# Kernel tuning notes

Hardware: AMD Instinct MI355X
Metric: run time of the kernel (lower is better)

Reference implementation:

```python
import jax, jax.numpy as jnp
import numpy as np

# ---- constants from init_kwargs (mode='local', channel='G') ----
MEAN = 127.5
STD = 50.0
BINS = np.array([-2.4, -1.6, -0.8, 0.0, 0.8, 1.6, 2.4])
NB = len(BINS) + 1            # 8 quantization levels
DIST = [1, 2, 3]
THETA = [0.0, np.pi / 4, np.pi / 2, 3 * np.pi / 4]
MASK = 17
STRIDE = 4
BIN_EDGES = 0.5 + BINS / 6.0
# skimage greycomatrix offsets: (round(sin(t)*d), round(cos(t)*d)), ordered d-major
OFFSETS = [(int(np.round(np.sin(t) * d)), int(np.round(np.cos(t) * d)))
           for d in DIST for t in THETA]


def setup_inputs() -> dict:
    key = jax.random.key(0)
    x = jax.random.uniform(key, (8, 3, 256, 256), dtype=jnp.float32) * 255.0
    return {"x": x}


def _features(x):
    img = x[:, 1, :, :]                       # channel 'G'
    img = jnp.where(img < 10.0, 0.0, img)     # imgs[imgs < 10] = 0
    B, H, W = img.shape
    N = (H - MASK) // STRIDE + 1              # 60 windows per axis

    # sliding windows -> (B, N, N, MASK, MASK)
    r = (jnp.arange(N) * STRIDE)[:, None] + jnp.arange(MASK)[None, :]
    win = img[:, r[:, None, :, None], r[None, :, None, :]]
    Nw = B * N * N
    flat = win.reshape(Nw, MASK * MASK)

    # ---- stat over nonzero pixels (numpy population std) ----
    mask = flat != 0.0
    n_safe = jnp.maximum(mask.sum(-1), 1).astype(flat.dtype)
    mean = jnp.where(mask, flat, 0.0).sum(-1) / n_safe
    std = jnp.sqrt((jnp.where(mask, flat - mean[:, None], 0.0) ** 2).sum(-1) / n_safe)
    mx = jnp.where(mask, flat, -jnp.inf).max(-1)
    mn = jnp.where(mask, flat, jnp.inf).min(-1)
    stat = jnp.stack([mean, std, (mx - mean) / (std + 1e-9), (mean - mn) / (std + 1e-9)], -1)

    # ---- quantize ----
    q = jnp.digitize(((flat - MEAN) / STD + 3.0) / 6.0, jnp.asarray(BIN_EDGES, flat.dtype))

    # ---- histogram (density over ALL pixels, drop first & last bin) ----
    onehot = (q[..., None] == jnp.arange(NB)).astype(flat.dtype)
    hist_feat = onehot.sum(1)[:, 1:NB - 1] / flat.shape[1]   # (Nw, len(BINS)-1)

    # ---- GLCM per (dist, theta) offset, symmetric + normed ----
    qm = q.reshape(Nw, MASK, MASK)
    rows = jnp.arange(Nw)[:, None]
    glcms = []
    for dr, dc in OFFSETS:
        if dc >= 0:
            i = qm[:, :MASK - dr, :MASK - dc]
            j = qm[:, dr:, dc:]
        else:
            i = qm[:, :MASK - dr, -dc:]
            j = qm[:, dr:, :MASK + dc]
        pair = (i * NB + j).reshape(Nw, -1)
        cnt = jnp.zeros((Nw, NB * NB), flat.dtype).at[rows, pair].add(1.0)
        P = cnt.reshape(Nw, NB, NB)
        P = P + P.transpose(0, 2, 1)                               # symmetric
        P = P / jnp.maximum(P.sum((1, 2), keepdims=True), 1e-12)   # normed
        glcms.append(P)
    G = jnp.stack(glcms, 1)          # (Nw, 12, NB, NB)
    g = G[:, :, 1:, 1:]              # crop level 0 (zeros)
    L = NB - 1

    # greycoprops renormalizes the (cropped) GLCM internally
    Pn = g / jnp.maximum(g.sum((2, 3), keepdims=True), 1e-12)
    I = jnp.arange(L, dtype=flat.dtype)
    diff2 = (I[:, None] - I[None, :]) ** 2
    contrast = (Pn * diff2).sum((2, 3))
    homog = (Pn / (1.0 + diff2)).sum((2, 3))
    energy = jnp.sqrt((Pn ** 2).sum((2, 3)))
    Pi = Pn.sum(3)
    Pj = Pn.sum(2)
    mui = (Pi * I).sum(-1)
    muj = (Pj * I).sum(-1)
    sdi = jnp.sqrt((Pi * (I - mui[..., None]) ** 2).sum(-1))
    sdj = jnp.sqrt((Pj * (I - muj[..., None]) ** 2).sum(-1))
    cov = (Pn * (I[:, None] - mui[..., None, None]) * (I[None, :] - muj[..., None, None])).sum((2, 3))
    corr = jnp.where(sdi * sdj < 1e-15, 1.0, cov / jnp.maximum(sdi * sdj, 1e-15))
    entropy = -(g * jnp.log2(g + 1e-8)).sum((2, 3))   # on cropped, non-renormed g

    glcm_feat = jnp.concatenate([contrast, homog, energy, corr, entropy], -1)  # (Nw, 60)
    feats = jnp.concatenate([stat, hist_feat, glcm_feat], -1)                  # (Nw, 70)

    # windows with max == 0 yield all-zero feature vectors
    feats = jnp.where((flat.max(-1) == 0.0)[:, None], 0.0, feats)

    Fdim = feats.shape[-1]
    feats = feats.reshape(B, N, N, Fdim)
    total = feats.sum((1, 2))
    nz = (feats != 0).sum((1, 2)).astype(flat.dtype)
    return total / (nz + 1e-9)            # (B, 70)


def reference(x):
    return _features(x)
```

## Files before the change

kernel.cpp:

```cpp
#include <hip/hip_runtime.h>
#include <cmath>

#define NPIX   289
#define NU     10
#define NF     70
#define NWX    60
#define IMG_W  256
#define IMG_HW 65536
#define NWIN   28800
#define ACC    560
#define WPB    2
#define NBLK   (NWIN / WPB)
#define GLS    29

__device__ __constant__ int c_s2u[12] = {0,1,2,3,4,1,5,3,6,7,8,9};

constexpr int JOFF[NU] = {1, 18, 17, 16, 2, 34, 3, 36, 51, 32};
constexpr float INV2N[NU] = {1.f/544.f, 1.f/512.f, 1.f/544.f, 1.f/512.f, 1.f/510.f,
                             1.f/510.f, 1.f/476.f, 1.f/450.f, 1.f/476.f, 1.f/450.f};

struct CMs { unsigned m[10]; };
constexpr CMs mkcm(int dc) {
    CMs c{};
    for (int t = 0; t < NPIX; ++t) {
        int col = t % 17;
        bool ok = (dc > 0) ? (col >= dc) : (col <= 16 + dc);
        if (ok) c.m[t >> 5] |= 1u << (t & 31);
    }
    return c;
}
constexpr CMs CMp1 = mkcm(1), CMp2 = mkcm(2), CMp3 = mkcm(3);
constexpr CMs CMn1 = mkcm(-1), CMn2 = mkcm(-2);

struct alignas(32) FtE { float w, d2, inv, si, sii, sij, q0, q1; };
struct FtTab { FtE e[28]; };
constexpr FtTab mkft() {
    FtTab t{};
    int n = 0;
    for (int a = 1; a <= 7; ++a)
        for (int b = a; b <= 7; ++b) {
            int i = a - 1, j = b - 1;
            float w  = (a == b) ? 1.f : 2.f;
            float d2 = (float)((i - j) * (i - j));
            t.e[n] = FtE{w, d2, 1.f / (1.f + d2),
                         0.5f * (float)(i + j),
                         0.5f * (float)(i * i + j * j),
                         (float)(i * j), 0.f, 0.f};
            ++n;
        }
    return t;
}
__device__ __constant__ FtTab c_ft = mkft();

template<int O>
__device__ __forceinline__ int gcnt(const unsigned* __restrict__ M,
                                    const unsigned* __restrict__ ma) {
    constexpr int wq = JOFF[O] >> 5;
    constexpr int rr = JOFF[O] & 31;
    constexpr int nw = (288 - JOFF[O]) / 32 + 1;
    int acc = 0;
#pragma unroll
    for (int w = 0; w < nw; ++w) {
        unsigned sh = (rr == 0) ? M[w + wq]
                                : __builtin_amdgcn_alignbit(M[w + wq + 1], M[w + wq], rr);
        acc += __popc(ma[w] & sh);
    }
    return acc;
}

#define DPP_F(oldv, srcv, ctrl, rm) \
    __int_as_float(__builtin_amdgcn_update_dpp((oldv), __float_as_int(srcv), (ctrl), (rm), 0xF, false))

__device__ __forceinline__ float dpp_wsum(float v) {
    v += DPP_F(0, v, 0x111, 0xF);
    v += DPP_F(0, v, 0x112, 0xF);
    v += DPP_F(0, v, 0x114, 0xF);
    v += DPP_F(0, v, 0x118, 0xF);
    v += DPP_F(0, v, 0x142, 0xA);
    v += DPP_F(0, v, 0x143, 0xC);
    return __int_as_float(__builtin_amdgcn_readlane(__float_as_int(v), 63));
}
__device__ __forceinline__ float dpp_wmax(float v) {
    v = fmaxf(v, DPP_F(__float_as_int(v), v, 0x111, 0xF));
    v = fmaxf(v, DPP_F(__float_as_int(v), v, 0x112, 0xF));
    v = fmaxf(v, DPP_F(__float_as_int(v), v, 0x114, 0xF));
    v = fmaxf(v, DPP_F(__float_as_int(v), v, 0x118, 0xF));
    v = fmaxf(v, DPP_F(__float_as_int(v), v, 0x142, 0xA));
    v = fmaxf(v, DPP_F(__float_as_int(v), v, 0x143, 0xC));
    return __int_as_float(__builtin_amdgcn_readlane(__float_as_int(v), 63));
}
__device__ __forceinline__ float dpp_wmin(float v) {
    v = fminf(v, DPP_F(__float_as_int(v), v, 0x111, 0xF));
    v = fminf(v, DPP_F(__float_as_int(v), v, 0x112, 0xF));
    v = fminf(v, DPP_F(__float_as_int(v), v, 0x114, 0xF));
    v = fminf(v, DPP_F(__float_as_int(v), v, 0x118, 0xF));
    v = fminf(v, DPP_F(__float_as_int(v), v, 0x142, 0xA));
    v = fminf(v, DPP_F(__float_as_int(v), v, 0x143, 0xC));
    return __int_as_float(__builtin_amdgcn_readlane(__float_as_int(v), 63));
}

__device__ __forceinline__ float bperm_f(int addr, float v) {
    return __int_as_float(__builtin_amdgcn_ds_bpermute(addr, __float_as_int(v)));
}

__global__ __launch_bounds__(128, 8) void feat_kernel(const float* __restrict__ x,
                                                      float* __restrict__ ptot,
                                                      float* __restrict__ pnz,
                                                      int setmask) {
    __shared__ float s_g[WPB][NU * GLS];
    __shared__ float s_uf[WPB][5][NU];
    __shared__ float s_s10[WPB][10];

    const int lane = threadIdx.x & 63;
    const int wid  = threadIdx.x >> 6;
    const int widx = blockIdx.x * WPB + wid;
    const int b    = widx / 3600;
    const int rem  = widx - b * 3600;
    const int wy   = rem / NWX;
    const int wx   = rem - wy * NWX;
    const float* img = x + (size_t)(b * 3 + 1) * IMG_HW + (wy * 4) * IMG_W + wx * 4;

    float* gl  = s_g[wid];
    float (*uf)[NU] = s_uf[wid];
    float* s10 = s_s10[wid];

    const int l49 = (lane < 49) ? lane : 48;
    const int ba  = l49 / 7 + 1;
    const int bb  = l49 - (ba - 1) * 7 + 1;
    const int partner = (bb - 1) * 7 + (ba - 1);
    const int paddr   = partner << 2;
    const unsigned long long xm0a = (ba & 1) ? 0ull : ~0ull;
    const unsigned long long xm1a = (ba & 2) ? 0ull : ~0ull;
    const unsigned long long xm2a = (ba & 4) ? 0ull : ~0ull;

    float lsum = 0.f, lss = 0.f, lmax = -1e30f, lmin = 1e30f;
    int n = 0, c1 = 0, c2 = 0, c3 = 0, c4 = 0, c5 = 0, c6 = 0;
    unsigned ma32[10];
#pragma unroll
    for (int k = 0; k < 5; ++k) {
        const int t = lane + k * 64;
        float val;
        if (k < 4) {
            const int r = t / 17;
            float p = img[r * (IMG_W - 17) + t];
            val = (p < 10.f) ? 0.f : p;
        } else {
            float p = 0.f;
            if (t < NPIX) {
                const int r = t / 17;
                p = img[r * (IMG_W - 17) + t];
            }
            val = (p < 10.f) ? 0.f : p;
        }
        int qq = (int)fmaf(val, 0.025f, 0.8125f);
        lsum += val;
        float d = (val != 0.f) ? (val - 127.5f) : 0.f;
        lss = fmaf(d, d, lss);
        lmax = fmaxf(lmax, val);
        lmin = fminf(lmin, (val != 0.f) ? val : 1e30f);
        unsigned long long p0 = __ballot(qq & 1);
        unsigned long long p1 = __ballot(qq & 2);
        unsigned long long p2 = __ballot(qq & 4);
        n  += __popcll(p0 | p1 | p2);
        c1 += __popcll(p0 & ~p1 & ~p2);
        c2 += __popcll(~p0 & p1 & ~p2);
        c3 += __popcll(p0 & p1 & ~p2);
        c4 += __popcll(~p0 & ~p1 & p2);
        c5 += __popcll(p0 & ~p1 & p2);
        c6 += __popcll(~p0 & p1 & p2);
        unsigned long long mA = (p0 ^ xm0a) & (p1 ^ xm1a) & (p2 ^ xm2a);
        ma32[2*k]   = (unsigned)mA;
        ma32[2*k+1] = (unsigned)(mA >> 32);
    }

    if (n == 0) return;

    unsigned mv0[10];
#pragma unroll
    for (int w = 0; w < 10; ++w)
        mv0[w] = (unsigned)__builtin_amdgcn_ds_bpermute(paddr, (int)ma32[w]);

    const float fn   = (float)n;
    const float sum  = dpp_wsum(lsum);
    const float ss   = dpp_wsum(lss);
    const float mx   = dpp_wmax(lmax);
    const float mn   = dpp_wmin(lmin);
    const float mean = sum / fn;
    const float mc   = mean - 127.5f;
    const float var  = fmaxf(ss / fn - mc * mc, 0.f);
    const float stdv = sqrtf(var);

    if (lane == 0) {
        s10[0] = mean;
        s10[1] = stdv;
        s10[2] = (mx - mean) / (stdv + 1e-9f);
        s10[3] = (mean - mn) / (stdv + 1e-9f);
        s10[4] = (float)c1 * (1.f / 289.f);
        s10[5] = (float)c2 * (1.f / 289.f);
        s10[6] = (float)c3 * (1.f / 289.f);
        s10[7] = (float)c4 * (1.f / 289.f);
        s10[8] = (float)c5 * (1.f / 289.f);
        s10[9] = (float)c6 * (1.f / 289.f);
    }

    int cnta[NU];
    {
        cnta[2] = gcnt<2>(mv0, ma32);
        cnta[5] = gcnt<5>(mv0, ma32);
        cnta[8] = gcnt<8>(mv0, ma32);
        unsigned mv[10];
#pragma unroll
        for (int w = 0; w < 10; ++w) mv[w] = mv0[w] & CMp1.m[w];
        cnta[0] = gcnt<0>(mv, ma32);
        cnta[1] = gcnt<1>(mv, ma32);
#pragma unroll
        for (int w = 0; w < 10; ++w) mv[w] = mv0[w] & CMp2.m[w];
        cnta[4] = gcnt<4>(mv, ma32);
        cnta[7] = gcnt<7>(mv, ma32);
#pragma unroll
        for (int w = 0; w < 10; ++w) mv[w] = mv0[w] & CMp3.m[w];
        cnta[6] = gcnt<6>(mv, ma32);
#pragma unroll
        for (int w = 0; w < 10; ++w) mv[w] = mv0[w] & CMn1.m[w];
        cnta[3] = gcnt<3>(mv, ma32);
#pragma unroll
        for (int w = 0; w < 10; ++w) mv[w] = mv0[w] & CMn2.m[w];
        cnta[9] = gcnt<9>(mv, ma32);
    }

    const int amin  = min(ba, bb);
    const int idx28 = 8 * (amin - 1) - ((amin * (amin - 1)) >> 1) + (max(ba, bb) - amin);
    const bool wr   = (lane < 49) && (ba <= bb);
#pragma unroll
    for (int o = 0; o < NU; ++o) {
        int pc = __builtin_amdgcn_ds_bpermute(paddr, cnta[o]);
        float g = (float)(cnta[o] + pc) * INV2N[o];
        if (wr) gl[o * GLS + idx28] = g;
    }

    const int fo  = lane & 15;
    const int sub = lane >> 4;
    float gsum=0.f, entU=0.f, conU=0.f, homU=0.f, g2=0.f, siU=0.f, siiU=0.f, sijU=0.f;
    if (fo < NU) {
#pragma unroll
        for (int i = 0; i < 7; ++i) {
            const int e = sub + 4 * i;
            FtE c = c_ft.e[e];
            float g  = gl[fo * GLS + e];
            float gw = g * c.w;
            float l  = __log2f(g + 1e-8f);
            gsum += gw;
            entU  = fmaf(gw, l,      entU);
            conU  = fmaf(gw, c.d2,   conU);
            homU  = fmaf(gw, c.inv,  homU);
            g2    = fmaf(gw, g,      g2);
            siU   = fmaf(gw, c.si,   siU);
            siiU  = fmaf(gw, c.sii,  siiU);
            sijU  = fmaf(gw, c.sij,  sijU);
        }
    }
    const int xa16 = (lane ^ 16) << 2;
    const int xa32 = (lane ^ 32) << 2;
    gsum += bperm_f(xa16, gsum);  entU += bperm_f(xa16, entU);
    conU += bperm_f(xa16, conU);  homU += bperm_f(xa16, homU);
    g2   += bperm_f(xa16, g2);    siU  += bperm_f(xa16, siU);
    siiU += bperm_f(xa16, siiU);  sijU += bperm_f(xa16, sijU);
    gsum += bperm_f(xa32, gsum);  entU += bperm_f(xa32, entU);
    conU += bperm_f(xa32, conU);  homU += bperm_f(xa32, homU);
    g2   += bperm_f(xa32, g2);    siU  += bperm_f(xa32, siU);
    siiU += bperm_f(xa32, siiU);  sijU += bperm_f(xa32, sijU);

    if (fo < NU && sub == 0) {
        const float invg = 1.f / fmaxf(gsum, 1e-12f);
        const float si  = siU  * invg;
        const float sii = siiU * invg;
        const float sij = sijU * invg;
        const float varg = fmaxf(sii - si * si, 0.f);
        const float cov  = sij - si * si;
        uf[0][fo] = conU * invg;
        uf[1][fo] = homU * invg;
        uf[2][fo] = sqrtf(g2) * invg;
        uf[3][fo] = (varg < 1e-15f) ? 1.f : cov / fmaxf(varg, 1e-15f);
        uf[4][fo] = -entU;
    }

    const int setbase = (widx & setmask) * ACC;
    const int obase   = b * NF;
    for (int t = lane; t < NF; t += 64) {
        float f;
        if (t < 10) {
            f = s10[t];
        } else {
            int u    = t - 10;
            int grp  = u / 12;
            int slot = u - grp * 12;
            f = uf[grp][c_s2u[slot]];
        }
        atomicAdd(&ptot[setbase + obase + t], f);
        if (t >= 4 && t <= 9 && f != 0.f)
            atomicAdd(&pnz[setbase + obase + t], 1.f);
    }
    if (lane == 0)
        atomicAdd(&pnz[setbase + obase], 1.f);
}

__global__ void reduce_kernel(const float* __restrict__ ptot,
                              const float* __restrict__ pnz,
                              float* __restrict__ out, int nset) {
    int t = blockIdx.x * blockDim.x + threadIdx.x;
    if (t >= ACC) return;
    int b = t / NF;
    int u = t - b * NF;
    bool hist = (u >= 4 && u <= 9);
    int nzidx = hist ? t : b * NF;
    float s = 0.f, nz = 0.f;
    for (int k = 0; k < nset; ++k) {
        s  += ptot[(size_t)k * ACC + t];
        nz += pnz[(size_t)k * ACC + nzidx];
    }
    out[t] = s / (nz + 1e-9f);
}

extern "C" void kernel_launch(void* const* d_in, const int* in_sizes, int n_in,
                              void* d_out, int out_size, void* d_ws, size_t ws_size,
                              hipStream_t stream) {
    (void)in_sizes; (void)n_in; (void)out_size;
    const float* x = (const float*)d_in[0];
    float* out = (float*)d_out;

    const size_t per_set = (size_t)2 * ACC * sizeof(float);
    int maxs = (ws_size >= per_set) ? (int)(ws_size / per_set) : 1;
    int nset = 1;
    while ((nset * 2) <= maxs && nset < 64) nset <<= 1;

    float* ptot = (float*)d_ws;
    float* pnz  = ptot + (size_t)nset * ACC;

    hipMemsetAsync(d_ws, 0, (size_t)nset * per_set, stream);
    feat_kernel<<<dim3(NBLK), dim3(WPB * 64), 0, stream>>>(x, ptot, pnz, nset - 1);
    reduce_kernel<<<dim3((ACC + 255) / 256), dim3(256), 0, stream>>>(ptot, pnz, out, nset);
}
```

Before: 113.7 us.

## Process four windows per wave with double-buffered loads and padded accumulators

Each wavefront now handles four horizontally adjacent windows. The next window's 289 pixels are prefetched into a second register buffer while the current one is processed, which hides global load latency and amortises per-wave setup such as lane partner indices. Blocks are interleaved across the batch via blockIdx&7, and the per-batch accumulator stride is padded from 70 to 80 floats to spread the atomics. The cost is four times fewer blocks, more registers for two load buffers, and a longer serial chain per wave, which could hurt occupancy or tail balance.

```diff
diff --git a/kernel.cpp b/kernel.cpp
--- a/kernel.cpp
+++ b/kernel.cpp
@@ -4,13 +4,16 @@
 #define NPIX   289
 #define NU     10
 #define NF     70
+#define NFP    80
 #define NWX    60
 #define IMG_W  256
 #define IMG_HW 65536
 #define NWIN   28800
 #define ACC    560
+#define ACCP   640
 #define WPB    2
-#define NBLK   (NWIN / WPB)
+#define WPW    4
+#define NBLK   (NWIN / (WPB * WPW))
 #define GLS    29
 
 __device__ __constant__ int c_s2u[12] = {0,1,2,3,4,1,5,3,6,7,8,9};
@@ -113,12 +116,13 @@
 
     const int lane = threadIdx.x & 63;
     const int wid  = threadIdx.x >> 6;
-    const int widx = blockIdx.x * WPB + wid;
-    const int b    = widx / 3600;
-    const int rem  = widx - b * 3600;
-    const int wy   = rem / NWX;
-    const int wx   = rem - wy * NWX;
-    const float* img = x + (size_t)(b * 3 + 1) * IMG_HW + (wy * 4) * IMG_W + wx * 4;
+    const int b     = blockIdx.x & 7;
+    const int lbid  = blockIdx.x >> 3;
+    const int rem0  = lbid * (WPB * WPW) + wid * WPW;
+    const int wy    = rem0 / NWX;
+    const int wx0   = rem0 - wy * NWX;
+    const int widx0 = b * 3600 + rem0;
+    const float* img0 = x + (size_t)(b * 3 + 1) * IMG_HW + (wy * 4) * IMG_W + wx0 * 4;
 
     float* gl  = s_g[wid];
     float (*uf)[NU] = s_uf[wid];
@@ -132,176 +136,192 @@
     const unsigned long long xm0a = (ba & 1) ? 0ull : ~0ull;
     const unsigned long long xm1a = (ba & 2) ? 0ull : ~0ull;
     const unsigned long long xm2a = (ba & 4) ? 0ull : ~0ull;
-
-    float lsum = 0.f, lss = 0.f, lmax = -1e30f, lmin = 1e30f;
-    int n = 0, c1 = 0, c2 = 0, c3 = 0, c4 = 0, c5 = 0, c6 = 0;
-    unsigned ma32[10];
-#pragma unroll
-    for (int k = 0; k < 5; ++k) {
-        const int t = lane + k * 64;
-        float val;
-        if (k < 4) {
-            const int r = t / 17;
-            float p = img[r * (IMG_W - 17) + t];
-            val = (p < 10.f) ? 0.f : p;
-        } else {
-            float p = 0.f;
-            if (t < NPIX) {
-                const int r = t / 17;
-                p = img[r * (IMG_W - 17) + t];
-            }
-            val = (p < 10.f) ? 0.f : p;
-        }
-        int qq = (int)fmaf(val, 0.025f, 0.8125f);
-        lsum += val;
-        float d = (val != 0.f) ? (val - 127.5f) : 0.f;
-        lss = fmaf(d, d, lss);
-        lmax = fmaxf(lmax, val);
-        lmin = fminf(lmin, (val != 0.f) ? val : 1e30f);
-        unsigned long long p0 = __ballot(qq & 1);
-        unsigned long long p1 = __ballot(qq & 2);
-        unsigned long long p2 = __ballot(qq & 4);
-        n  += __popcll(p0 | p1 | p2);
-        c1 += __popcll(p0 & ~p1 & ~p2);
-        c2 += __popcll(~p0 & p1 & ~p2);
-        c3 += __popcll(p0 & p1 & ~p2);
-        c4 += __popcll(~p0 & ~p1 & p2);
-        c5 += __popcll(p0 & ~p1 & p2);
-        c6 += __popcll(~p0 & p1 & p2);
-        unsigned long long mA = (p0 ^ xm0a) & (p1 ^ xm1a) & (p2 ^ xm2a);
-        ma32[2*k]   = (unsigned)mA;
-        ma32[2*k+1] = (unsigned)(mA >> 32);
-    }
-
-    if (n == 0) return;
-
-    unsigned mv0[10];
-#pragma unroll
-    for (int w = 0; w < 10; ++w)
-        mv0[w] = (unsigned)__builtin_amdgcn_ds_bpermute(paddr, (int)ma32[w]);
-
-    const float fn   = (float)n;
-    const float sum  = dpp_wsum(lsum);
-    const float ss   = dpp_wsum(lss);
-    const float mx   = dpp_wmax(lmax);
-    const float mn   = dpp_wmin(lmin);
-    const float mean = sum / fn;
-    const float mc   = mean - 127.5f;
-    const float var  = fmaxf(ss / fn - mc * mc, 0.f);
-    const float stdv = sqrtf(var);
-
-    if (lane == 0) {
-        s10[0] = mean;
-        s10[1] = stdv;
-        s10[2] = (mx - mean) / (stdv + 1e-9f);
-        s10[3] = (mean - mn) / (stdv + 1e-9f);
-        s10[4] = (float)c1 * (1.f / 289.f);
-        s10[5] = (float)c2 * (1.f / 289.f);
-        s10[6] = (float)c3 * (1.f / 289.f);
-        s10[7] = (float)c4 * (1.f / 289.f);
-        s10[8] = (float)c5 * (1.f / 289.f);
-        s10[9] = (float)c6 * (1.f / 289.f);
-    }
-
-    int cnta[NU];
-    {
-        cnta[2] = gcnt<2>(mv0, ma32);
-        cnta[5] = gcnt<5>(mv0, ma32);
-        cnta[8] = gcnt<8>(mv0, ma32);
-        unsigned mv[10];
-#pragma unroll
-        for (int w = 0; w < 10; ++w) mv[w] = mv0[w] & CMp1.m[w];
-        cnta[0] = gcnt<0>(mv, ma32);
-        cnta[1] = gcnt<1>(mv, ma32);
-#pragma unroll
-        for (int w = 0; w < 10; ++w) mv[w] = mv0[w] & CMp2.m[w];
-        cnta[4] = gcnt<4>(mv, ma32);
-        cnta[7] = gcnt<7>(mv, ma32);
-#pragma unroll
-        for (int w = 0; w < 10; ++w) mv[w] = mv0[w] & CMp3.m[w];
-        cnta[6] = gcnt<6>(mv, ma32);
-#pragma unroll
-        for (int w = 0; w < 10; ++w) mv[w] = mv0[w] & CMn1.m[w];
-        cnta[3] = gcnt<3>(mv, ma32);
-#pragma unroll
-        for (int w = 0; w < 10; ++w) mv[w] = mv0[w] & CMn2.m[w];
-        cnta[9] = gcnt<9>(mv, ma32);
-    }
-
     const int amin  = min(ba, bb);
     const int idx28 = 8 * (amin - 1) - ((amin * (amin - 1)) >> 1) + (max(ba, bb) - amin);
     const bool wr   = (lane < 49) && (ba <= bb);
-#pragma unroll
-    for (int o = 0; o < NU; ++o) {
-        int pc = __builtin_amdgcn_ds_bpermute(paddr, cnta[o]);
-        float g = (float)(cnta[o] + pc) * INV2N[o];
-        if (wr) gl[o * GLS + idx28] = g;
-    }
-
     const int fo  = lane & 15;
     const int sub = lane >> 4;
-    float gsum=0.f, entU=0.f, conU=0.f, homU=0.f, g2=0.f, siU=0.f, siiU=0.f, sijU=0.f;
-    if (fo < NU) {
-#pragma unroll
-        for (int i = 0; i < 7; ++i) {
-            const int e = sub + 4 * i;
-            FtE c = c_ft.e[e];
-            float g  = gl[fo * GLS + e];
-            float gw = g * c.w;
-            float l  = __log2f(g + 1e-8f);
-            gsum += gw;
-            entU  = fmaf(gw, l,      entU);
-            conU  = fmaf(gw, c.d2,   conU);
-            homU  = fmaf(gw, c.inv,  homU);
-            g2    = fmaf(gw, g,      g2);
-            siU   = fmaf(gw, c.si,   siU);
-            siiU  = fmaf(gw, c.sii,  siiU);
-            sijU  = fmaf(gw, c.sij,  sijU);
-        }
-    }
     const int xa16 = (lane ^ 16) << 2;
     const int xa32 = (lane ^ 32) << 2;
-    gsum += bperm_f(xa16, gsum);  entU += bperm_f(xa16, entU);
-    conU += bperm_f(xa16, conU);  homU += bperm_f(xa16, homU);
-    g2   += bperm_f(xa16, g2);    siU  += bperm_f(xa16, siU);
-    siiU += bperm_f(xa16, siiU);  sijU += bperm_f(xa16, sijU);
-    gsum += bperm_f(xa32, gsum);  entU += bperm_f(xa32, entU);
-    conU += bperm_f(xa32, conU);  homU += bperm_f(xa32, homU);
-    g2   += bperm_f(xa32, g2);    siU  += bperm_f(xa32, siU);
-    siiU += bperm_f(xa32, siiU);  sijU += bperm_f(xa32, sijU);
-
-    if (fo < NU && sub == 0) {
-        const float invg = 1.f / fmaxf(gsum, 1e-12f);
-        const float si  = siU  * invg;
-        const float sii = siiU * invg;
-        const float sij = sijU * invg;
-        const float varg = fmaxf(sii - si * si, 0.f);
-        const float cov  = sij - si * si;
-        uf[0][fo] = conU * invg;
-        uf[1][fo] = homU * invg;
-        uf[2][fo] = sqrtf(g2) * invg;
-        uf[3][fo] = (varg < 1e-15f) ? 1.f : cov / fmaxf(varg, 1e-15f);
-        uf[4][fo] = -entU;
+    const int obase = b * NFP;
+
+    int off[5];
+#pragma unroll
+    for (int k = 0; k < 5; ++k) {
+        int t = lane + k * 64;
+        int r = t / 17;
+        off[k] = r * (IMG_W - 17) + t;
     }
-
-    const int setbase = (widx & setmask) * ACC;
-    const int obase   = b * NF;
-    for (int t = lane; t < NF; t += 64) {
-        float f;
-        if (t < 10) {
-            f = s10[t];
-        } else {
-            int u    = t - 10;
-            int grp  = u / 12;
-            int slot = u - grp * 12;
-            f = uf[grp][c_s2u[slot]];
-        }
-        atomicAdd(&ptot[setbase + obase + t], f);
-        if (t >= 4 && t <= 9 && f != 0.f)
-            atomicAdd(&pnz[setbase + obase + t], 1.f);
-    }
-    if (lane == 0)
-        atomicAdd(&pnz[setbase + obase], 1.f);
+    const bool v4 = (lane < NPIX - 256);
+
+    auto PROC = [&](const float (&pv)[5], int widx) {
+        float lsum = 0.f, lss = 0.f, lmax = -1e30f, lmin = 1e30f;
+        int n = 0, c1 = 0, c2 = 0, c3 = 0, c4 = 0, c5 = 0, c6 = 0;
+        unsigned ma32[10];
+#pragma unroll
+        for (int k = 0; k < 5; ++k) {
+            float p = pv[k];
+            float val = (p < 10.f) ? 0.f : p;
+            if (k == 4) val = v4 ? val : 0.f;
+            int qq = (int)fmaf(val, 0.025f, 0.8125f);
+            lsum += val;
+            float d = (val != 0.f) ? (val - 127.5f) : 0.f;
+            lss = fmaf(d, d, lss);
+            lmax = fmaxf(lmax, val);
+            lmin = fminf(lmin, (val != 0.f) ? val : 1e30f);
+            unsigned long long p0 = __ballot(qq & 1);
+            unsigned long long p1 = __ballot(qq & 2);
+            unsigned long long p2 = __ballot(qq & 4);
+            n  += __popcll(p0 | p1 | p2);
+            c1 += __popcll(p0 & ~p1 & ~p2);
+            c2 += __popcll(~p0 & p1 & ~p2);
+            c3 += __popcll(p0 & p1 & ~p2);
+            c4 += __popcll(~p0 & ~p1 & p2);
+            c5 += __popcll(p0 & ~p1 & p2);
+            c6 += __popcll(~p0 & p1 & p2);
+            unsigned long long mA = (p0 ^ xm0a) & (p1 ^ xm1a) & (p2 ^ xm2a);
+            ma32[2*k]   = (unsigned)mA;
+            ma32[2*k+1] = (unsigned)(mA >> 32);
+        }
+
+        if (n == 0) return;
+
+        unsigned mv0[10];
+#pragma unroll
+        for (int w = 0; w < 10; ++w)
+            mv0[w] = (unsigned)__builtin_amdgcn_ds_bpermute(paddr, (int)ma32[w]);
+
+        const float fn   = (float)n;
+        const float sum  = dpp_wsum(lsum);
+        const float ss   = dpp_wsum(lss);
+        const float mx   = dpp_wmax(lmax);
+        const float mn   = dpp_wmin(lmin);
+        const float mean = sum / fn;
+        const float mc   = mean - 127.5f;
+        const float var  = fmaxf(ss / fn - mc * mc, 0.f);
+        const float stdv = sqrtf(var);
+
+        if (lane == 0) {
+            s10[0] = mean;
+            s10[1] = stdv;
+            s10[2] = (mx - mean) / (stdv + 1e-9f);
+            s10[3] = (mean - mn) / (stdv + 1e-9f);
+            s10[4] = (float)c1 * (1.f / 289.f);
+            s10[5] = (float)c2 * (1.f / 289.f);
+            s10[6] = (float)c3 * (1.f / 289.f);
+            s10[7] = (float)c4 * (1.f / 289.f);
+            s10[8] = (float)c5 * (1.f / 289.f);
+            s10[9] = (float)c6 * (1.f / 289.f);
+        }
+
+        int cnta[NU];
+        {
+            cnta[2] = gcnt<2>(mv0, ma32);
+            cnta[5] = gcnt<5>(mv0, ma32);
+            cnta[8] = gcnt<8>(mv0, ma32);
+            unsigned mv[10];
+#pragma unroll
+            for (int w = 0; w < 10; ++w) mv[w] = mv0[w] & CMp1.m[w];
+            cnta[0] = gcnt<0>(mv, ma32);
+            cnta[1] = gcnt<1>(mv, ma32);
+#pragma unroll
+            for (int w = 0; w < 10; ++w) mv[w] = mv0[w] & CMp2.m[w];
+            cnta[4] = gcnt<4>(mv, ma32);
+            cnta[7] = gcnt<7>(mv, ma32);
+#pragma unroll
+            for (int w = 0; w < 10; ++w) mv[w] = mv0[w] & CMp3.m[w];
+            cnta[6] = gcnt<6>(mv, ma32);
+#pragma unroll
+            for (int w = 0; w < 10; ++w) mv[w] = mv0[w] & CMn1.m[w];
+            cnta[3] = gcnt<3>(mv, ma32);
+#pragma unroll
+            for (int w = 0; w < 10; ++w) mv[w] = mv0[w] & CMn2.m[w];
+            cnta[9] = gcnt<9>(mv, ma32);
+        }
+
+#pragma unroll
+        for (int o = 0; o < NU; ++o) {
+            int pc = __builtin_amdgcn_ds_bpermute(paddr, cnta[o]);
+            float g = (float)(cnta[o] + pc) * INV2N[o];
+            if (wr) gl[o * GLS + idx28] = g;
+        }
+
+        float gsum=0.f, entU=0.f, conU=0.f, homU=0.f, g2=0.f, siU=0.f, siiU=0.f, sijU=0.f;
+        if (fo < NU) {
+#pragma unroll
+            for (int i = 0; i < 7; ++i) {
+                const int e = sub + 4 * i;
+                FtE c = c_ft.e[e];
+                float g  = gl[fo * GLS + e];
+                float gw = g * c.w;
+                float l  = __log2f(g + 1e-8f);
+                gsum += gw;
+                entU  = fmaf(gw, l,      entU);
+                conU  = fmaf(gw, c.d2,   conU);
+                homU  = fmaf(gw, c.inv,  homU);
+                g2    = fmaf(gw, g,      g2);
+                siU   = fmaf(gw, c.si,   siU);
+                siiU  = fmaf(gw, c.sii,  siiU);
+                sijU  = fmaf(gw, c.sij,  sijU);
+            }
+        }
+        gsum += bperm_f(xa16, gsum);  entU += bperm_f(xa16, entU);
+        conU += bperm_f(xa16, conU);  homU += bperm_f(xa16, homU);
+        g2   += bperm_f(xa16, g2);    siU  += bperm_f(xa16, siU);
+        siiU += bperm_f(xa16, siiU);  sijU += bperm_f(xa16, sijU);
+        gsum += bperm_f(xa32, gsum);  entU += bperm_f(xa32, entU);
+        conU += bperm_f(xa32, conU);  homU += bperm_f(xa32, homU);
+        g2   += bperm_f(xa32, g2);    siU  += bperm_f(xa32, siU);
+        siiU += bperm_f(xa32, siiU);  sijU += bperm_f(xa32, sijU);
+
+        if (fo < NU && sub == 0) {
+            const float invg = 1.f / fmaxf(gsum, 1e-12f);
+            const float si  = siU  * invg;
+            const float sii = siiU * invg;
+            const float sij = sijU * invg;
+            const float varg = fmaxf(sii - si * si, 0.f);
+            const float cov  = sij - si * si;
+            uf[0][fo] = conU * invg;
+            uf[1][fo] = homU * invg;
+            uf[2][fo] = sqrtf(g2) * invg;
+            uf[3][fo] = (varg < 1e-15f) ? 1.f : cov / fmaxf(varg, 1e-15f);
+            uf[4][fo] = -entU;
+        }
+
+        const int setbase = (widx & setmask) * ACCP;
+        for (int t = lane; t < NF; t += 64) {
+            float f;
+            if (t < 10) {
+                f = s10[t];
+            } else {
+                int u    = t - 10;
+                int grp  = u / 12;
+                int slot = u - grp * 12;
+                f = uf[grp][c_s2u[slot]];
+            }
+            atomicAdd(&ptot[setbase + obase + t], f);
+            if (t >= 4 && t <= 9 && f != 0.f)
+                atomicAdd(&pnz[setbase + obase + t], 1.f);
+        }
+        if (lane == 0)
+            atomicAdd(&pnz[setbase + obase], 1.f);
+    };
+
+#define LOADW(buf, iw) { \
+        const float* ip = img0 + (iw) * 4; \
+        buf[0] = ip[off[0]]; buf[1] = ip[off[1]]; buf[2] = ip[off[2]]; \
+        buf[3] = ip[off[3]]; buf[4] = ip[off[4]]; }
+
+    float bufA[5], bufB[5];
+    LOADW(bufA, 0)
+    LOADW(bufB, 1)
+    PROC(bufA, widx0 + 0);
+    LOADW(bufA, 2)
+    PROC(bufB, widx0 + 1);
+    LOADW(bufB, 3)
+    PROC(bufA, widx0 + 2);
+    PROC(bufB, widx0 + 3);
+#undef LOADW
 }
 
 __global__ void reduce_kernel(const float* __restrict__ ptot,
@@ -311,12 +331,13 @@
     if (t >= ACC) return;
     int b = t / NF;
     int u = t - b * NF;
+    int pa = b * NFP + u;
     bool hist = (u >= 4 && u <= 9);
-    int nzidx = hist ? t : b * NF;
+    int nzidx = hist ? pa : b * NFP;
     float s = 0.f, nz = 0.f;
     for (int k = 0; k < nset; ++k) {
-        s  += ptot[(size_t)k * ACC + t];
-        nz += pnz[(size_t)k * ACC + nzidx];
+        s  += ptot[(size_t)k * ACCP + pa];
+        nz += pnz[(size_t)k * ACCP + nzidx];
     }
     out[t] = s / (nz + 1e-9f);
 }
@@ -328,13 +349,13 @@
     const float* x = (const float*)d_in[0];
     float* out = (float*)d_out;
 
-    const size_t per_set = (size_t)2 * ACC * sizeof(float);
+    const size_t per_set = (size_t)2 * ACCP * sizeof(float);
     int maxs = (ws_size >= per_set) ? (int)(ws_size / per_set) : 1;
     int nset = 1;
     while ((nset * 2) <= maxs && nset < 64) nset <<= 1;
 
     float* ptot = (float*)d_ws;
-    float* pnz  = ptot + (size_t)nset * ACC;
+    float* pnz  = ptot + (size_t)nset * ACCP;
 
     hipMemsetAsync(d_ws, 0, (size_t)nset * per_set, stream);
     feat_kernel<<<dim3(NBLK), dim3(WPB * 64), 0, stream>>>(x, ptot, pnz, nset - 1);
```

Result: slower. 136.7 us (+20.2%).
